# Kernel tuning notes

Hardware: AMD Instinct MI355X
Metric: run time of the kernel (lower is better)

The kernel has to match this reference:

```python
import jax, jax.numpy as jnp
import numpy as np

K0 = 0.7978845608028654  # sqrt(2/pi)
C1 = 0.044715

def _gelu_tanh(x):
    # tanh-approx GELU, matching the Triton kernel's math
    return 0.5 * x * (1.0 + jnp.tanh(K0 * (x + C1 * x * x * x)))

def setup_inputs() -> dict:
    key = jax.random.key(0)
    k1, k2, k3 = jax.random.split(key, 3)
    B, C_in, H, W = 32, 64, 128, 128
    C_out, KH = 128, 3
    x = jax.random.normal(k1, (B, C_in, H, W), dtype=jnp.float32)
    weight = jax.random.normal(k2, (C_out, C_in, KH, KH), dtype=jnp.float32)
    bias = jax.random.normal(k3, (C_out,), dtype=jnp.float32)
    return {"x": x, "weight": weight, "bias": bias}

def reference(x, weight, bias):
    # Valid conv2d, stride 1 (NCHW, OIHW)
    y = jax.lax.conv_general_dilated(
        x, weight,
        window_strides=(1, 1), padding="VALID",
        dimension_numbers=("NCHW", "OIHW", "NCHW"))
    y = y + bias[None, :, None, None]
    y = _gelu_tanh(y)
    # global average pool over spatial dims -> [B, C_out]
    return jnp.mean(y, axis=(2, 3))
```

## Files before the change

kernel.cpp:

```cpp
#include <hip/hip_runtime.h>
#include <cstdint>
#include <cstddef>

#define GK0 0.7978845608028654f
#define GC1 0.044715f

typedef __attribute__((ext_vector_type(8))) short short8;
typedef __attribute__((ext_vector_type(4))) short short4v;
typedef __attribute__((ext_vector_type(4))) float floatx4;

__device__ __forceinline__ unsigned short f2bf(float f) {
  union { float f; unsigned int u; } v; v.f = f;
  unsigned int r = v.u + 0x7fffu + ((v.u >> 16) & 1u);
  return (unsigned short)(r >> 16);
}

__global__ void k_wt(const float* __restrict__ w, unsigned short* __restrict__ wt,
                     float* __restrict__ out) {
  if (blockIdx.x == 0) {
    for (int i = threadIdx.x; i < 32 * 128; i += 256) out[i] = 0.0f;
  }
  int t = blockIdx.x * 256 + threadIdx.x;
  if (t >= 128 * 64 * 9) return;
  int co = t / 576; int r = t - co * 576; int ci = r / 9; int khw = r - ci * 9;
  wt[(khw * 128 + co) * 64 + ci] = f2bf(w[t]);
}

__global__ __launch_bounds__(256, 2) void k_conv(
    const float* __restrict__ x, const unsigned short* __restrict__ wt,
    const float* __restrict__ bias, float* __restrict__ out) {
  __shared__ __align__(16) unsigned short xs[8 * 66 * 72];
  const int tid = threadIdx.x;
  const int b = blockIdx.z, hbase = blockIdx.y * 6, w0 = blockIdx.x * 64;
  const int lane = tid & 63, wave = tid >> 6;
  const int wm = wave & 1, wn = wave >> 1;
  const int m = lane & 15, q = lane >> 4;

  const float* xb = x + (size_t)b * 64 * 16384;
  const int g = tid >> 4, w4 = tid & 15;
  const int hci = tid & 63, hrow = tid >> 6;

  {
    const float* p0 = xb + (size_t)(4 * g) * 16384 + (size_t)hbase * 128 + w0 + 4 * w4;
    float4 rv[16];
#pragma unroll
    for (int row = 0; row < 4; row++)
#pragma unroll
      for (int c = 0; c < 4; c++)
        rv[row * 4 + c] = *(const float4*)(p0 + (size_t)c * 16384 + row * 128);
    float2 hv = make_float2(0.f, 0.f);
    if (w0 == 0) hv = *(const float2*)(xb + (size_t)hci * 16384 + (size_t)(hbase + hrow) * 128 + 64);
#pragma unroll
    for (int row = 0; row < 4; row++) {
      unsigned short* dr = xs + row * (66 * 72);
#pragma unroll
      for (int wj = 0; wj < 4; wj++) {
        short4v sv;
#pragma unroll
        for (int c = 0; c < 4; c++) sv[c] = (short)f2bf(((const float*)&rv[row * 4 + c])[wj]);
        *(short4v*)(dr + (4 * w4 + wj) * 72 + 4 * g) = sv;
      }
    }
    xs[hrow * (66 * 72) + 64 * 72 + hci] = f2bf(hv.x);
    xs[hrow * (66 * 72) + 65 * 72 + hci] = f2bf(hv.y);
  }
  __syncthreads();

  float bvv[4][4];
#pragma unroll
  for (int mt = 0; mt < 4; mt++)
#pragma unroll
    for (int r2 = 0; r2 < 4; r2++) bvv[mt][r2] = bias[wm * 64 + mt * 16 + q * 4 + r2];

  const unsigned short* wbase = wt + ((wm * 64 + m) * 64 + q * 8);
  int bb[4];
#pragma unroll
  for (int nt = 0; nt < 4; nt++) bb[nt] = (nt * 16 + m) * 72 + q * 8;

  float gsum[4][4];
#pragma unroll
  for (int i = 0; i < 4; i++)
#pragma unroll
    for (int j = 0; j < 4; j++) gsum[i][j] = 0.f;

  for (int t = 0; t < 3; t++) {
    const bool pre = (t < 2);
    floatx4 acc[4][4];
#pragma unroll
    for (int i = 0; i < 4; i++)
#pragma unroll
      for (int j = 0; j < 4; j++) acc[i][j] = (floatx4){0.f, 0.f, 0.f, 0.f};

    short8 a_cur[4], a_nxt[4];
#pragma unroll
    for (int mt = 0; mt < 4; mt++) a_cur[mt] = *(const short8*)(wbase + mt * 1024);

    float4 pr[8];
    float2 ph = make_float2(0.f, 0.f);

#pragma unroll
    for (int kk = 0; kk < 18; kk++) {
      const int khw = kk >> 1, cb = (kk & 1) << 5;
      const int kh = khw / 3, kw = khw - kh * 3;
      if (kk < 17) {
        const int khw2 = (kk + 1) >> 1, cb2 = ((kk + 1) & 1) << 5;
        const unsigned short* p = wbase + khw2 * 8192 + cb2;
#pragma unroll
        for (int mt = 0; mt < 4; mt++) a_nxt[mt] = *(const short8*)(p + mt * 1024);
      }
      short8 bf[4];
      const int off = ((2 * t + wn + kh) * 66 + kw) * 72 + cb;
#pragma unroll
      for (int nt = 0; nt < 4; nt++) bf[nt] = *(const short8*)(&xs[bb[nt] + off]);
#pragma unroll
      for (int mt = 0; mt < 4; mt++)
#pragma unroll
        for (int nt = 0; nt < 4; nt++)
          acc[mt][nt] = __builtin_amdgcn_mfma_f32_16x16x32_bf16(a_cur[mt], bf[nt], acc[mt][nt], 0, 0, 0);
      if (kk == 8 && pre) {
        const int prow = hbase + 4 + 2 * t;
        const float* pp = xb + (size_t)(4 * g) * 16384 + (size_t)prow * 128 + w0 + 4 * w4;
#pragma unroll
        for (int rr = 0; rr < 2; rr++)
#pragma unroll
          for (int c = 0; c < 4; c++)
            pr[rr * 4 + c] = *(const float4*)(pp + (size_t)c * 16384 + rr * 128);
        if (w0 == 0 && tid < 128)
          ph = *(const float2*)(xb + (size_t)hci * 16384 + (size_t)(prow + (hrow & 1)) * 128 + 64);
      }
#pragma unroll
      for (int mt = 0; mt < 4; mt++) a_cur[mt] = a_nxt[mt];
    }

#pragma unroll
    for (int mt = 0; mt < 4; mt++)
#pragma unroll
      for (int r2 = 0; r2 < 4; r2++) {
        float s = 0.f;
#pragma unroll
        for (int nt = 0; nt < 4; nt++) {
          float y = acc[mt][nt][r2] + bvv[mt][r2];
          float u = GK0 * (y + GC1 * y * y * y);
          float e = __expf(-2.0f * u);
          float gg = y * __builtin_amdgcn_rcpf(1.0f + e);
          if (w0 + nt * 16 + m < 126) s += gg;
        }
        gsum[mt][r2] += s;
      }

    if (pre) {
      const int s0 = 4 + 2 * t;
#pragma unroll
      for (int rr = 0; rr < 2; rr++) {
        unsigned short* dr = xs + (s0 + rr) * (66 * 72);
#pragma unroll
        for (int wj = 0; wj < 4; wj++) {
          short4v sv;
#pragma unroll
          for (int c = 0; c < 4; c++) sv[c] = (short)f2bf(((const float*)&pr[rr * 4 + c])[wj]);
          *(short4v*)(dr + (4 * w4 + wj) * 72 + 4 * g) = sv;
        }
      }
      if (tid < 128) {
        unsigned short* dr = xs + (s0 + (hrow & 1)) * (66 * 72);
        dr[64 * 72 + hci] = f2bf(ph.x);
        dr[65 * 72 + hci] = f2bf(ph.y);
      }
    }
    __syncthreads();
  }

  const float inv_area = 1.0f / (126.0f * 126.0f);
  float* orow = out + b * 128;
#pragma unroll
  for (int mt = 0; mt < 4; mt++)
#pragma unroll
    for (int r2 = 0; r2 < 4; r2++) {
      float s = gsum[mt][r2];
#pragma unroll
      for (int d = 1; d < 16; d <<= 1) s += __shfl_xor(s, d, 64);
      if (m == 0) atomicAdd(&orow[wm * 64 + mt * 16 + q * 4 + r2], s * inv_area);
    }
}

extern "C" void kernel_launch(void* const* d_in, const int* in_sizes, int n_in,
                              void* d_out, int out_size, void* d_ws, size_t ws_size,
                              hipStream_t stream) {
  const float* x    = (const float*)d_in[0];
  const float* w    = (const float*)d_in[1];
  const float* bias = (const float*)d_in[2];
  float* out = (float*)d_out;

  unsigned short* wbuf = (unsigned short*)d_ws;
  if (ws_size < (size_t)9 * 128 * 64 * 2) return;

  k_wt<<<288, 256, 0, stream>>>(w, wbuf, out);
  k_conv<<<dim3(2, 21, 32), 256, 0, stream>>>(x, wbuf, bias, out);
}
```

Measured before the change: 458.0 us.

## Switch conv to full-width row tiles with 4-slot ring buffer and XOR-swizzled LDS

Each block now covers the full 128-wide row span and 8 output rows, using a 4-row ring buffer in shared memory that holds one input row per slot as [w][ci] bf16 with an XOR swizzle instead of padding. The next input row is loaded into registers before the MFMA loop and written to LDS afterward. This removes the halo column handling and the duplicate row loads between the old 64-wide, 6-row blocks, and it avoids bank conflicts without padding. In exchange the grid is smaller (512 blocks), the row loop is longer and more serial, and the global loads are scalar per channel rather than float4.

```diff
diff --git a/kernel.cpp b/kernel.cpp
--- a/kernel.cpp
+++ b/kernel.cpp
@@ -6,7 +6,6 @@
 #define GC1 0.044715f
 
 typedef __attribute__((ext_vector_type(8))) short short8;
-typedef __attribute__((ext_vector_type(4))) short short4v;
 typedef __attribute__((ext_vector_type(4))) float floatx4;
 
 __device__ __forceinline__ unsigned short f2bf(float f) {
@@ -29,40 +28,33 @@
 __global__ __launch_bounds__(256, 2) void k_conv(
     const float* __restrict__ x, const unsigned short* __restrict__ wt,
     const float* __restrict__ bias, float* __restrict__ out) {
-  __shared__ __align__(16) unsigned short xs[8 * 66 * 72];
+  __shared__ __align__(16) unsigned short xs[4 * 8192];
   const int tid = threadIdx.x;
-  const int b = blockIdx.z, hbase = blockIdx.y * 6, w0 = blockIdx.x * 64;
+  const int r0 = blockIdx.x * 8, b = blockIdx.y;
+  const int L = min(8, 126 - r0);
   const int lane = tid & 63, wave = tid >> 6;
   const int wm = wave & 1, wn = wave >> 1;
   const int m = lane & 15, q = lane >> 4;
+  const float* xb32 = x + (size_t)b * 64 * 16384;
+  const int wsp = tid & 127, oh = tid >> 7;
 
-  const float* xb = x + (size_t)b * 64 * 16384;
-  const int g = tid >> 4, w4 = tid & 15;
-  const int hci = tid & 63, hrow = tid >> 6;
 
-  {
-    const float* p0 = xb + (size_t)(4 * g) * 16384 + (size_t)hbase * 128 + w0 + 4 * w4;
-    float4 rv[16];
+  for (int rr = 0; rr < 3; rr++) {
+    const float* src = xb32 + (size_t)(r0 + rr) * 128 + wsp;
+    float pf[32];
 #pragma unroll
-    for (int row = 0; row < 4; row++)
+    for (int g = 0; g < 4; g++)
 #pragma unroll
-      for (int c = 0; c < 4; c++)
-        rv[row * 4 + c] = *(const float4*)(p0 + (size_t)c * 16384 + row * 128);
-    float2 hv = make_float2(0.f, 0.f);
-    if (w0 == 0) hv = *(const float2*)(xb + (size_t)hci * 16384 + (size_t)(hbase + hrow) * 128 + 64);
+      for (int j = 0; j < 8; j++)
+        pf[g * 8 + j] = src[(size_t)((oh * 4 + g) * 8 + j) * 16384];
 #pragma unroll
-    for (int row = 0; row < 4; row++) {
-      unsigned short* dr = xs + row * (66 * 72);
+    for (int g = 0; g < 4; g++) {
+      const int oct = oh * 4 + g;
+      short8 sv;
 #pragma unroll
-      for (int wj = 0; wj < 4; wj++) {
-        short4v sv;
-#pragma unroll
-        for (int c = 0; c < 4; c++) sv[c] = (short)f2bf(((const float*)&rv[row * 4 + c])[wj]);
-        *(short4v*)(dr + (4 * w4 + wj) * 72 + 4 * g) = sv;
-      }
+      for (int j = 0; j < 8; j++) sv[j] = (short)f2bf(pf[g * 8 + j]);
+      *(short8*)&xs[rr * 8192 + wsp * 64 + ((oct ^ (wsp & 7)) << 3)] = sv;
     }
-    xs[hrow * (66 * 72) + 64 * 72 + hci] = f2bf(hv.x);
-    xs[hrow * (66 * 72) + 65 * 72 + hci] = f2bf(hv.y);
   }
   __syncthreads();
 
@@ -73,18 +65,24 @@
     for (int r2 = 0; r2 < 4; r2++) bvv[mt][r2] = bias[wm * 64 + mt * 16 + q * 4 + r2];
 
   const unsigned short* wbase = wt + ((wm * 64 + m) * 64 + q * 8);
-  int bb[4];
-#pragma unroll
-  for (int nt = 0; nt < 4; nt++) bb[nt] = (nt * 16 + m) * 72 + q * 8;
-
   float gsum[4][4];
 #pragma unroll
   for (int i = 0; i < 4; i++)
 #pragma unroll
     for (int j = 0; j < 4; j++) gsum[i][j] = 0.f;
 
-  for (int t = 0; t < 3; t++) {
-    const bool pre = (t < 2);
+  for (int t = 0; t < L; t++) {
+    const bool pre = (t < L - 1);
+    float pf[32];
+    if (pre) {
+      const float* src = xb32 + (size_t)(r0 + t + 3) * 128 + wsp;
+#pragma unroll
+      for (int g = 0; g < 4; g++)
+#pragma unroll
+        for (int j = 0; j < 8; j++)
+          pf[g * 8 + j] = src[(size_t)((oh * 4 + g) * 8 + j) * 16384];
+    }
+
     floatx4 acc[4][4];
 #pragma unroll
     for (int i = 0; i < 4; i++)
@@ -95,12 +93,11 @@
 #pragma unroll
     for (int mt = 0; mt < 4; mt++) a_cur[mt] = *(const short8*)(wbase + mt * 1024);
 
-    float4 pr[8];
-    float2 ph = make_float2(0.f, 0.f);
+    const int sbs[3] = {(t & 3) * 8192, ((t + 1) & 3) * 8192, ((t + 2) & 3) * 8192};
 
 #pragma unroll
     for (int kk = 0; kk < 18; kk++) {
-      const int khw = kk >> 1, cb = (kk & 1) << 5;
+      const int khw = kk >> 1, half = kk & 1;
       const int kh = khw / 3, kw = khw - kh * 3;
       if (kk < 17) {
         const int khw2 = (kk + 1) >> 1, cb2 = ((kk + 1) & 1) << 5;
@@ -108,28 +105,30 @@
 #pragma unroll
         for (int mt = 0; mt < 4; mt++) a_nxt[mt] = *(const short8*)(p + mt * 1024);
       }
+      const int swz = ((q + 4 * half) ^ ((m + kw) & 7)) << 3;
+      const int base = sbs[kh] + (wn * 64 + m + kw) * 64 + swz;
       short8 bf[4];
-      const int off = ((2 * t + wn + kh) * 66 + kw) * 72 + cb;
 #pragma unroll
-      for (int nt = 0; nt < 4; nt++) bf[nt] = *(const short8*)(&xs[bb[nt] + off]);
+      for (int nt = 0; nt < 4; nt++) bf[nt] = *(const short8*)&xs[base + nt * 1024];
 #pragma unroll
       for (int mt = 0; mt < 4; mt++)
 #pragma unroll
         for (int nt = 0; nt < 4; nt++)
           acc[mt][nt] = __builtin_amdgcn_mfma_f32_16x16x32_bf16(a_cur[mt], bf[nt], acc[mt][nt], 0, 0, 0);
-      if (kk == 8 && pre) {
-        const int prow = hbase + 4 + 2 * t;
-        const float* pp = xb + (size_t)(4 * g) * 16384 + (size_t)prow * 128 + w0 + 4 * w4;
-#pragma unroll
-        for (int rr = 0; rr < 2; rr++)
-#pragma unroll
-          for (int c = 0; c < 4; c++)
-            pr[rr * 4 + c] = *(const float4*)(pp + (size_t)c * 16384 + rr * 128);
-        if (w0 == 0 && tid < 128)
-          ph = *(const float2*)(xb + (size_t)hci * 16384 + (size_t)(prow + (hrow & 1)) * 128 + 64);
-      }
 #pragma unroll
       for (int mt = 0; mt < 4; mt++) a_cur[mt] = a_nxt[mt];
+    }
+
+    if (pre) {
+      unsigned short* dst = &xs[((t + 3) & 3) * 8192];
+#pragma unroll
+      for (int g = 0; g < 4; g++) {
+        const int oct = oh * 4 + g;
+        short8 sv;
+#pragma unroll
+        for (int j = 0; j < 8; j++) sv[j] = (short)f2bf(pf[g * 8 + j]);
+        *(short8*)&dst[wsp * 64 + ((oct ^ (wsp & 7)) << 3)] = sv;
+      }
     }
 
 #pragma unroll
@@ -143,30 +142,11 @@
           float u = GK0 * (y + GC1 * y * y * y);
           float e = __expf(-2.0f * u);
           float gg = y * __builtin_amdgcn_rcpf(1.0f + e);
-          if (w0 + nt * 16 + m < 126) s += gg;
+          if (wn * 64 + nt * 16 + m < 126) s += gg;
         }
         gsum[mt][r2] += s;
       }
 
-    if (pre) {
-      const int s0 = 4 + 2 * t;
-#pragma unroll
-      for (int rr = 0; rr < 2; rr++) {
-        unsigned short* dr = xs + (s0 + rr) * (66 * 72);
-#pragma unroll
-        for (int wj = 0; wj < 4; wj++) {
-          short4v sv;
-#pragma unroll
-          for (int c = 0; c < 4; c++) sv[c] = (short)f2bf(((const float*)&pr[rr * 4 + c])[wj]);
-          *(short4v*)(dr + (4 * w4 + wj) * 72 + 4 * g) = sv;
-        }
-      }
-      if (tid < 128) {
-        unsigned short* dr = xs + (s0 + (hrow & 1)) * (66 * 72);
-        dr[64 * 72 + hci] = f2bf(ph.x);
-        dr[65 * 72 + hci] = f2bf(ph.y);
-      }
-    }
     __syncthreads();
   }
 
@@ -195,5 +175,5 @@
   if (ws_size < (size_t)9 * 128 * 64 * 2) return;
 
   k_wt<<<288, 256, 0, stream>>>(w, wbuf, out);
-  k_conv<<<dim3(2, 21, 32), 256, 0, stream>>>(x, wbuf, bias, out);
+  k_conv<<<dim3(16, 32), 256, 0, stream>>>(x, wbuf, bias, out);
 }
```

Result: slower. 595.9 us (+30.1%).
